# Performance work log

Measured on AMD Instinct MI355X. Metric: run time of the kernel, lower is better.

## Reference

```python
import jax, jax.numpy as jnp
import numpy as np

N_EMBD = 1024
HEAD_SIZE = 128


def setup_inputs() -> dict:
    key = jax.random.key(0)
    k_x, k_w, k_cov, k_b = jax.random.split(key, 4)
    x = jax.random.normal(k_x, (16384, 2, N_EMBD), dtype=jnp.float32)
    # values_proj: nn.Linear(n_embd, head_size, bias=False) -> weight [head_size, n_embd]
    W = jax.random.normal(k_w, (HEAD_SIZE, N_EMBD), dtype=jnp.float32) * (N_EMBD ** -0.5)
    cov = jax.random.normal(k_cov, (HEAD_SIZE, HEAD_SIZE), dtype=jnp.float32) * (HEAD_SIZE ** -0.5)
    bias = jax.random.normal(k_b, (HEAD_SIZE,), dtype=jnp.float32)
    return {"x": x, "W": W, "cov": cov, "bias": bias}


def reference(x, W, cov, bias):
    # x: [B, 2, E]; W: [H, E]; cov: [H, H]; bias: [H]
    values = jnp.einsum('be,he->bh', x[:, 0, :], W)  # [B, H]
    mask = jnp.einsum('be,he->bh', x[:, 1, :], W)    # [B, H]
    # diag_embed(mask) @ cov == mask[:, :, None] * cov  -> [B, H, H]
    coeffs = jax.nn.softmax(mask[:, :, None] * cov[None, :, :], axis=-1)
    # values.unsqueeze(1) @ coeffs + bias, then [:, 0, :]
    out = jnp.einsum('bh,bhk->bk', values, coeffs) + bias
    return out
```

## Files before the change

### kernel.cpp

```cpp
#include <hip/hip_runtime.h>

#define LOG2E 1.4426950408889634f

typedef __attribute__((ext_vector_type(8))) short frag_ab;
typedef __attribute__((ext_vector_type(4))) float frag_cd;

__device__ inline short f2bf(float f) {
    union { float f; unsigned u; } v; v.f = f;
    unsigned r = v.u + 0x7fffu + ((v.u >> 16) & 1u);
    return (short)(r >> 16);
}

template<int CTRL>
__device__ inline float dpp_ror_add(float x) {
    int t = __builtin_amdgcn_update_dpp(0, __builtin_bit_cast(int, x), CTRL, 0xf, 0xf, false);
    return x + __builtin_bit_cast(float, t);
}

#define PACK_AF(af, p0, p1)                                                   \
    af[0] = f2bf(p0.x); af[1] = f2bf(p0.y); af[2] = f2bf(p0.z); af[3] = f2bf(p0.w); \
    af[4] = f2bf(p1.x); af[5] = f2bf(p1.y); af[6] = f2bf(p1.z); af[7] = f2bf(p1.w);

__global__ __launch_bounds__(256) void prep_kernel(const float* __restrict__ W,
                                                   short* __restrict__ wbf) {
    int g = blockIdx.x * 256 + threadIdx.x;
    int h = g >> 7;
    int k0 = (g & 127) << 3;
    const float* src = W + h * 1024 + k0;
    float4 w0 = *(const float4*)src;
    float4 w1 = *(const float4*)(src + 4);
    frag_ab af;
    PACK_AF(af, w0, w1);
    int c = k0 >> 6, s = (k0 >> 5) & 1, kg = (k0 >> 3) & 3;
    int nt = h >> 4, m = h & 15, lane = kg * 16 + m;
    int dst = (((c * 8 + nt) * 2 + s) * 64 + lane) * 8;
    *(frag_ab*)(wbf + dst) = af;
}

__global__ __launch_bounds__(256, 4) void proj_kernel(const float* __restrict__ x,
                                                      const short* __restrict__ wbf,
                                                      float* __restrict__ vm) {
    const int tid = threadIdx.x;
    const int lane = tid & 63, wave = tid >> 6;
    const int m = lane & 15, kg = lane >> 4;
    const long rowbase = (long)blockIdx.x * 64 + wave * 16;
    const float* xrow = x + (rowbase + m) * 1024 + kg * 8;
    const frag_ab* wb = (const frag_ab*)wbf + lane;

    frag_cd acc[8];
#pragma unroll
    for (int nt = 0; nt < 8; ++nt) acc[nt] = (frag_cd){0.f, 0.f, 0.f, 0.f};

    float4 a0 = *(const float4*)(xrow);
    float4 a1 = *(const float4*)(xrow + 4);
    float4 a2 = *(const float4*)(xrow + 32);
    float4 a3 = *(const float4*)(xrow + 36);

    for (int c = 0; c < 16; ++c) {
        float4 n0, n1, n2, n3;
        if (c < 15) {
            const float* xn = xrow + (c + 1) * 64;
            n0 = *(const float4*)(xn);
            n1 = *(const float4*)(xn + 4);
            n2 = *(const float4*)(xn + 32);
            n3 = *(const float4*)(xn + 36);
        }
        frag_ab af0, af1;
        PACK_AF(af0, a0, a1);
        PACK_AF(af1, a2, a3);

        const frag_ab* bp = wb + (size_t)c * 1024;
#pragma unroll
        for (int nt = 0; nt < 8; ++nt) {
            frag_ab bf0 = bp[(nt * 2 + 0) * 64];
            acc[nt] = __builtin_amdgcn_mfma_f32_16x16x32_bf16(af0, bf0, acc[nt], 0, 0, 0);
            frag_ab bf1 = bp[(nt * 2 + 1) * 64];
            acc[nt] = __builtin_amdgcn_mfma_f32_16x16x32_bf16(af1, bf1, acc[nt], 0, 0, 0);
        }
        if (c < 15) { a0 = n0; a1 = n1; a2 = n2; a3 = n3; }
    }

#pragma unroll
    for (int nt = 0; nt < 8; ++nt)
#pragma unroll
        for (int r = 0; r < 4; ++r) {
            long row = rowbase + kg * 4 + r;
            vm[row * 128 + nt * 16 + m] = acc[nt][r];
        }
}

__global__ __launch_bounds__(512, 6) void combine_kernel(const float* __restrict__ vm,
                                                         const float* __restrict__ cov,
                                                         const float* __restrict__ bias,
                                                         float* __restrict__ out) {
    __shared__ float obuf[2][32][132];

    const int t = threadIdx.x;
    const int i = t >> 4;
    const int j = t & 15;
    const float bias_own = bias[t & 127];

    float covreg[4][8];
#pragma unroll
    for (int hh = 0; hh < 4; ++hh) {
        const float* cr = cov + (long)(i * 4 + hh) * 128 + j * 8;
        float4 c0 = *(const float4*)cr;
        float4 c1 = *(const float4*)(cr + 4);
        covreg[hh][0] = LOG2E * c0.x; covreg[hh][1] = LOG2E * c0.y;
        covreg[hh][2] = LOG2E * c0.z; covreg[hh][3] = LOG2E * c0.w;
        covreg[hh][4] = LOG2E * c1.x; covreg[hh][5] = LOG2E * c1.y;
        covreg[hh][6] = LOG2E * c1.z; covreg[hh][7] = LOG2E * c1.w;
    }

    const long b0 = (long)blockIdx.x * 8;
    for (int rr = 0; rr < 4; ++rr) {
#pragma unroll
        for (int sb = 0; sb < 2; ++sb) {
            const long b = b0 + rr * 2 + sb;
            float4 v4 = *(const float4*)(vm + (2 * b) * 128 + i * 4);
            float4 m4 = *(const float4*)(vm + (2 * b + 1) * 128 + i * 4);
            float vh[4] = {v4.x, v4.y, v4.z, v4.w};
            float mh[4] = {m4.x, m4.y, m4.z, m4.w};
            float op[8] = {0.f, 0.f, 0.f, 0.f, 0.f, 0.f, 0.f, 0.f};
#pragma unroll
            for (int hh = 0; hh < 4; ++hh) {
                float mv = mh[hh];
                float p[8];
#pragma unroll
                for (int kk = 0; kk < 8; ++kk)
                    p[kk] = __builtin_amdgcn_exp2f(mv * covreg[hh][kk]);
                float s0 = p[0] + p[1], s1 = p[2] + p[3];
                float s2 = p[4] + p[5], s3 = p[6] + p[7];
                float lsum = (s0 + s1) + (s2 + s3);
                lsum = dpp_ror_add<0x121>(lsum);
                lsum = dpp_ror_add<0x122>(lsum);
                lsum = dpp_ror_add<0x124>(lsum);
                lsum = dpp_ror_add<0x128>(lsum);
                float w = vh[hh] * __builtin_amdgcn_rcpf(lsum);
#pragma unroll
                for (int kk = 0; kk < 8; ++kk) op[kk] = fmaf(w, p[kk], op[kk]);
            }
            *(float4*)&obuf[sb][i][j * 8]     = make_float4(op[0], op[1], op[2], op[3]);
            *(float4*)&obuf[sb][i][j * 8 + 4] = make_float4(op[4], op[5], op[6], op[7]);
        }
        __syncthreads();
        if (t < 256) {
            const int k  = t & 127;
            const int sb = t >> 7;
            float o = bias_own;
#pragma unroll
            for (int ii = 0; ii < 32; ++ii) o += obuf[sb][ii][k];
            out[(b0 + rr * 2 + sb) * 128 + k] = o;
        }
        __syncthreads();
    }
}

extern "C" void kernel_launch(void* const* d_in, const int* in_sizes, int n_in,
                              void* d_out, int out_size, void* d_ws, size_t ws_size,
                              hipStream_t stream) {
    const float* x    = (const float*)d_in[0];
    const float* W    = (const float*)d_in[1];
    const float* cov  = (const float*)d_in[2];
    const float* bias = (const float*)d_in[3];
    float* out = (float*)d_out;

    const int B = in_sizes[0] / (2 * 1024);

    short* wbf = (short*)d_ws;
    float* vm  = (float*)(wbf + 128 * 1024);

    prep_kernel<<<64, 256, 0, stream>>>(W, wbf);
    proj_kernel<<<(2 * B) / 64, 256, 0, stream>>>(x, wbf, vm);
    combine_kernel<<<B / 8, 512, 0, stream>>>(vm, cov, bias, out);
}
```

Before: 310.3 us.

## Stage x tiles into LDS via direct global-to-LDS loads; batch four rows in combine

The projection kernel now stages x into a 64x260 float LDS tile (about 66KB) using global_load_lds in four quarter-K phases. Each wave then reads its MFMA A fragments from LDS instead of from strided per-lane global loads with register prefetch. The aim is coalesced, full-row global reads and fewer register-held prefetches, but it drops occupancy to 2 blocks and adds barriers with no double buffering. The combine kernel processes four batch rows per iteration instead of two, so all 512 threads do the final reduction and half as many barriers are needed, at the cost of more LDS per block.

```diff
diff --git a/kernel.cpp b/kernel.cpp
--- a/kernel.cpp
+++ b/kernel.cpp
@@ -16,6 +16,10 @@
     int t = __builtin_amdgcn_update_dpp(0, __builtin_bit_cast(int, x), CTRL, 0xf, 0xf, false);
     return x + __builtin_bit_cast(float, t);
 }
+
+#define GLD_TO_LDS(gp, lp)                                                              \
+    __builtin_amdgcn_global_load_lds((const __attribute__((address_space(1))) void*)(gp), \
+                                     (__attribute__((address_space(3))) void*)(lp), 16, 0, 0)
 
 #define PACK_AF(af, p0, p1)                                                   \
     af[0] = f2bf(p0.x); af[1] = f2bf(p0.y); af[2] = f2bf(p0.z); af[3] = f2bf(p0.w); \
@@ -37,63 +41,68 @@
     *(frag_ab*)(wbf + dst) = af;
 }
 
-__global__ __launch_bounds__(256, 4) void proj_kernel(const float* __restrict__ x,
+__global__ __launch_bounds__(256, 2) void proj_kernel(const float* __restrict__ x,
                                                       const short* __restrict__ wbf,
                                                       float* __restrict__ vm) {
+    __shared__ __align__(16) float xs[64][260];
+
     const int tid = threadIdx.x;
     const int lane = tid & 63, wave = tid >> 6;
     const int m = lane & 15, kg = lane >> 4;
-    const long rowbase = (long)blockIdx.x * 64 + wave * 16;
-    const float* xrow = x + (rowbase + m) * 1024 + kg * 8;
+    const long rowbase = (long)blockIdx.x * 64;
     const frag_ab* wb = (const frag_ab*)wbf + lane;
 
     frag_cd acc[8];
 #pragma unroll
     for (int nt = 0; nt < 8; ++nt) acc[nt] = (frag_cd){0.f, 0.f, 0.f, 0.f};
 
-    float4 a0 = *(const float4*)(xrow);
-    float4 a1 = *(const float4*)(xrow + 4);
-    float4 a2 = *(const float4*)(xrow + 32);
-    float4 a3 = *(const float4*)(xrow + 36);
+    for (int q = 0; q < 4; ++q) {
+#pragma unroll
+        for (int i = 0; i < 16; ++i) {
+            const int r = 4 * i + wave;
+            const float* gp = x + (rowbase + r) * 1024 + q * 256 + lane * 4;
+            GLD_TO_LDS(gp, &xs[r][lane * 4]);
+        }
+        __syncthreads();
 
-    for (int c = 0; c < 16; ++c) {
-        float4 n0, n1, n2, n3;
-        if (c < 15) {
-            const float* xn = xrow + (c + 1) * 64;
-            n0 = *(const float4*)(xn);
-            n1 = *(const float4*)(xn + 4);
-            n2 = *(const float4*)(xn + 32);
-            n3 = *(const float4*)(xn + 36);
+#pragma unroll
+        for (int cl = 0; cl < 4; ++cl) {
+            const int c = q * 4 + cl;
+            const float* xr = &xs[wave * 16 + m][cl * 64 + kg * 8];
+            float4 a0 = *(const float4*)(xr);
+            float4 a1 = *(const float4*)(xr + 4);
+            float4 a2 = *(const float4*)(xr + 32);
+            float4 a3 = *(const float4*)(xr + 36);
+            frag_ab af0, af1;
+            PACK_AF(af0, a0, a1);
+            PACK_AF(af1, a2, a3);
+
+            const frag_ab* bp = wb + (size_t)c * 1024;
+#pragma unroll
+            for (int nt = 0; nt < 8; ++nt) {
+                frag_ab bf0 = bp[(nt * 2 + 0) * 64];
+                acc[nt] = __builtin_amdgcn_mfma_f32_16x16x32_bf16(af0, bf0, acc[nt], 0, 0, 0);
+                frag_ab bf1 = bp[(nt * 2 + 1) * 64];
+                acc[nt] = __builtin_amdgcn_mfma_f32_16x16x32_bf16(af1, bf1, acc[nt], 0, 0, 0);
+            }
         }
-        frag_ab af0, af1;
-        PACK_AF(af0, a0, a1);
-        PACK_AF(af1, a2, a3);
-
-        const frag_ab* bp = wb + (size_t)c * 1024;
-#pragma unroll
-        for (int nt = 0; nt < 8; ++nt) {
-            frag_ab bf0 = bp[(nt * 2 + 0) * 64];
-            acc[nt] = __builtin_amdgcn_mfma_f32_16x16x32_bf16(af0, bf0, acc[nt], 0, 0, 0);
-            frag_ab bf1 = bp[(nt * 2 + 1) * 64];
-            acc[nt] = __builtin_amdgcn_mfma_f32_16x16x32_bf16(af1, bf1, acc[nt], 0, 0, 0);
-        }
-        if (c < 15) { a0 = n0; a1 = n1; a2 = n2; a3 = n3; }
+        __syncthreads();
     }
 
 #pragma unroll
     for (int nt = 0; nt < 8; ++nt)
 #pragma unroll
         for (int r = 0; r < 4; ++r) {
-            long row = rowbase + kg * 4 + r;
+            long row = rowbase + wave * 16 + kg * 4 + r;
             vm[row * 128 + nt * 16 + m] = acc[nt][r];
         }
 }
 
-__global__ __launch_bounds__(512, 6) void combine_kernel(const float* __restrict__ vm,
+__global__ __launch_bounds__(512, 4) void combine_kernel(const float* __restrict__ vm,
                                                          const float* __restrict__ cov,
                                                          const float* __restrict__ bias,
                                                          float* __restrict__ out) {
-    __shared__ float obuf[2][32][132];
+    __shared__ float obuf[4][32][132];
 
     const int t = threadIdx.x;
     const int i = t >> 4;
@@ -113,10 +122,10 @@
     }
 
     const long b0 = (long)blockIdx.x * 8;
-    for (int rr = 0; rr < 4; ++rr) {
+    for (int rr = 0; rr < 2; ++rr) {
 #pragma unroll
-        for (int sb = 0; sb < 2; ++sb) {
-            const long b = b0 + rr * 2 + sb;
+        for (int sb = 0; sb < 4; ++sb) {
+            const long b = b0 + rr * 4 + sb;
             float4 v4 = *(const float4*)(vm + (2 * b) * 128 + i * 4);
             float4 m4 = *(const float4*)(vm + (2 * b + 1) * 128 + i * 4);
             float vh[4] = {v4.x, v4.y, v4.z, v4.w};
@@ -144,13 +153,13 @@
             *(float4*)&obuf[sb][i][j * 8 + 4] = make_float4(op[4], op[5], op[6], op[7]);
         }
         __syncthreads();
-        if (t < 256) {
+        {
             const int k  = t & 127;
             const int sb = t >> 7;
             float o = bias_own;
 #pragma unroll
             for (int ii = 0; ii < 32; ++ii) o += obuf[sb][ii][k];
-            out[(b0 + rr * 2 + sb) * 128 + k] = o;
+            out[(b0 + rr * 4 + sb) * 128 + k] = o;
         }
         __syncthreads();
     }
```

After: 291.1 us. 1.07x faster.
